# Kernel tuning notes

Hardware: AMD Instinct MI355X
Metric: run time of the kernel (lower is better)

## Reference

```python
import jax, jax.numpy as jnp
import numpy as np

TGT, SRC, BATCH, HID, ATT = 64, 64, 32, 512, 512

def setup_inputs() -> dict:
    key = jax.random.key(0)
    k1, k2, k3, k4 = jax.random.split(key, 4)
    h_t = jax.random.normal(k1, (TGT, BATCH, HID), dtype=jnp.float32)
    src_encodings = jax.random.normal(k2, (SRC, BATCH, HID), dtype=jnp.float32)
    # Wa: Linear(2*HID -> ATT, bias=False); stored as (in, out) for jnp.
    Wa = jax.random.normal(k3, (2 * HID, ATT), dtype=jnp.float32) * (1.0 / np.sqrt(2 * HID))
    # Va: Linear(ATT -> 1, bias=False)
    Va = jax.random.normal(k4, (ATT,), dtype=jnp.float32) * (1.0 / np.sqrt(ATT))
    return {"h_t": h_t, "src_encodings": src_encodings, "Wa": Wa, "Va": Va}

def reference(h_t, src_encodings, Wa, Va):
    # Wa([h_t, src]) = h_t @ Wa_h + src @ Wa_s (exact by linearity of concat-matmul)
    Wa_h, Wa_s = Wa[:HID], Wa[HID:]                 # (H, A) each
    h_part = jnp.einsum('tbh,ha->tba', h_t, Wa_h)   # (T, B, A)
    s_part = jnp.einsum('sbh,ha->sba', src_encodings, Wa_s)  # (S, B, A)
    # scores[s, t, b] = Va . tanh(h_part[t,b] + s_part[s,b])
    hidden = jnp.tanh(h_part[None, :, :, :] + s_part[:, None, :, :])  # (S, T, B, A)
    scores = jnp.einsum('stba,a->stb', hidden, Va)  # (S, T, B)
    attn = jax.nn.softmax(scores, axis=0)           # softmax over src dim
    # context[t,b,:] = sum_s attn[s,t,b] * src[s,b,:]
    context = jnp.einsum('stb,sbh->tbh', attn, src_encodings)  # (T, B, H)
    return context
```

## Files before the change

### kernel.cpp

```cpp
#include <hip/hip_runtime.h>
#include <hip/hip_bf16.h>

#define TGT   64
#define SRCN  64
#define BATCH 32
#define HID   512
#define ATT   512
#define MROWS (TGT * BATCH)

typedef __bf16 bf16_t;
typedef __bf16 bf16x8 __attribute__((ext_vector_type(8)));
typedef float  f32x4  __attribute__((ext_vector_type(4)));

__device__ __forceinline__ float fast_exp2(float x) {
#if __has_builtin(__builtin_amdgcn_exp2f)
  return __builtin_amdgcn_exp2f(x);
#else
  float r; asm("v_exp_f32 %0, %1\n\ts_nop 1" : "=v"(r) : "v"(x)); return r;
#endif
}
__device__ __forceinline__ float fast_rcp(float x) {
#if __has_builtin(__builtin_amdgcn_rcpf)
  return __builtin_amdgcn_rcpf(x);
#else
  float r; asm("v_rcp_f32 %0, %1\n\ts_nop 1" : "=v"(r) : "v"(x)); return r;
#endif
}

#define MFMA(a, b, c) __builtin_amdgcn_mfma_f32_16x16x32_bf16((a), (b), (c), 0, 0, 0)

__global__ __launch_bounds__(256) void proj_gemm(
    const float* __restrict__ h_t, const float* __restrict__ srcp,
    const float* __restrict__ Wa, float* __restrict__ C)
{
  const int z = blockIdx.z;
  const float* __restrict__ A = z ? srcp : h_t;
  const int mbase = blockIdx.x * 64;
  const int nbase = blockIdx.y * 64;

  __shared__ bf16_t Ah[64][72];
  __shared__ bf16_t Al[64][72];
  __shared__ bf16_t Bh[64][72];
  __shared__ bf16_t Bl[64][72];

  const int tid  = threadIdx.x;
  const int lane = tid & 63;
  const int wv   = tid >> 6;
  const int wm   = (wv & 1) * 32;
  const int wn   = (wv >> 1) * 32;
  const int l15  = lane & 15;
  const int qd   = lane >> 4;

  const int arow = tid >> 2;
  const int akc  = (tid & 3) * 16;
  const int bn = tid & 63;
  const int bkg = (tid >> 6) * 16;

  const float* Aptr = A + (size_t)(mbase + arow) * HID + akc;
  const float* Bptr = Wa + (size_t)(z * HID + bkg) * ATT + nbase + bn;

  f32x4 acc00 = {0.f, 0.f, 0.f, 0.f};
  f32x4 acc01 = acc00, acc10 = acc00, acc11 = acc00;

  for (int kb = 0; kb < HID; kb += 64) {
    if (kb) __syncthreads();

    {
      float4 a0 = *(const float4*)(Aptr + kb);
      float4 a1 = *(const float4*)(Aptr + kb + 4);
      float4 a2 = *(const float4*)(Aptr + kb + 8);
      float4 a3 = *(const float4*)(Aptr + kb + 12);
      float av[16] = {a0.x, a0.y, a0.z, a0.w, a1.x, a1.y, a1.z, a1.w,
                      a2.x, a2.y, a2.z, a2.w, a3.x, a3.y, a3.z, a3.w};
      bf16x8 hi0, hi1, lo0, lo1;
#pragma unroll
      for (int j = 0; j < 8; ++j) {
        bf16_t h = (bf16_t)av[j];
        hi0[j] = h;
        lo0[j] = (bf16_t)(av[j] - (float)h);
        bf16_t h2 = (bf16_t)av[j + 8];
        hi1[j] = h2;
        lo1[j] = (bf16_t)(av[j + 8] - (float)h2);
      }
      *(bf16x8*)&Ah[arow][akc]     = hi0;
      *(bf16x8*)&Ah[arow][akc + 8] = hi1;
      *(bf16x8*)&Al[arow][akc]     = lo0;
      *(bf16x8*)&Al[arow][akc + 8] = lo1;
    }

    {
      const float* bp = Bptr + (size_t)kb * ATT;
      float bv[16];
#pragma unroll
      for (int j = 0; j < 16; ++j) bv[j] = bp[(size_t)j * ATT];
      bf16x8 hi0, hi1, lo0, lo1;
#pragma unroll
      for (int j = 0; j < 8; ++j) {
        bf16_t h = (bf16_t)bv[j];
        hi0[j] = h;
        lo0[j] = (bf16_t)(bv[j] - (float)h);
        bf16_t h2 = (bf16_t)bv[j + 8];
        hi1[j] = h2;
        lo1[j] = (bf16_t)(bv[j + 8] - (float)h2);
      }
      *(bf16x8*)&Bh[bn][bkg]     = hi0;
      *(bf16x8*)&Bh[bn][bkg + 8] = hi1;
      *(bf16x8*)&Bl[bn][bkg]     = lo0;
      *(bf16x8*)&Bl[bn][bkg + 8] = lo1;
    }
    __syncthreads();

#pragma unroll
    for (int h = 0; h < 2; ++h) {
      const int kh = h * 32 + qd * 8;
      bf16x8 ah0 = *(const bf16x8*)&Ah[wm + l15][kh];
      bf16x8 ah1 = *(const bf16x8*)&Ah[wm + 16 + l15][kh];
      bf16x8 al0 = *(const bf16x8*)&Al[wm + l15][kh];
      bf16x8 al1 = *(const bf16x8*)&Al[wm + 16 + l15][kh];
      bf16x8 bh0 = *(const bf16x8*)&Bh[wn + l15][kh];
      bf16x8 bh1 = *(const bf16x8*)&Bh[wn + 16 + l15][kh];
      bf16x8 bl0 = *(const bf16x8*)&Bl[wn + l15][kh];
      bf16x8 bl1 = *(const bf16x8*)&Bl[wn + 16 + l15][kh];

      acc00 = MFMA(ah0, bh0, acc00);
      acc01 = MFMA(ah0, bh1, acc01);
      acc10 = MFMA(ah1, bh0, acc10);
      acc11 = MFMA(ah1, bh1, acc11);
      acc00 = MFMA(al0, bh0, acc00);
      acc01 = MFMA(al0, bh1, acc01);
      acc10 = MFMA(al1, bh0, acc10);
      acc11 = MFMA(al1, bh1, acc11);
      acc00 = MFMA(ah0, bl0, acc00);
      acc01 = MFMA(ah0, bl1, acc01);
      acc10 = MFMA(ah1, bl0, acc10);
      acc11 = MFMA(ah1, bl1, acc11);
    }
  }

  float* Cz = C + (size_t)z * (MROWS * ATT);
#pragma unroll
  for (int r = 0; r < 4; ++r) {
    int row0 = mbase + wm + qd * 4 + r;
    int row1 = row0 + 16;
    int col0 = nbase + wn + l15;
    Cz[(size_t)row0 * ATT + col0]      = acc00[r];
    Cz[(size_t)row0 * ATT + col0 + 16] = acc01[r];
    Cz[(size_t)row1 * ATT + col0]      = acc10[r];
    Cz[(size_t)row1 * ATT + col0 + 16] = acc11[r];
  }
}

__global__ __launch_bounds__(512) void attn_fused(
    const float* __restrict__ ws, const float* __restrict__ srcp,
    const float* __restrict__ Va, float* __restrict__ out)
{
  const float* __restrict__ h_part = ws;
  const float* __restrict__ s_part = ws + (size_t)TGT * BATCH * ATT;
  const float SC = 2.8853900817779268f;

  const int t0   = blockIdx.x * 4;
  const int b    = blockIdx.y;
  const int tid  = threadIdx.x;
  const int lane = tid & 63;
  const int wv   = tid >> 6;

  __shared__ float scoreLds[4][64];
  __shared__ float attnLds[4][64];

  const int abase = lane * 8;
  float va[8], H[4][8];
  *(float4*)&va[0] = *(const float4*)(Va + abase);
  *(float4*)&va[4] = *(const float4*)(Va + abase + 4);

  float vsum = 0.f;
#pragma unroll
  for (int j = 0; j < 8; ++j) vsum += va[j];
#pragma unroll
  for (int off = 32; off; off >>= 1) vsum += __shfl_xor(vsum, off);

#pragma unroll
  for (int t = 0; t < 4; ++t) {
    const float* hp = h_part + ((size_t)(t0 + t) * BATCH + b) * ATT + abase;
    float4 h0 = *(const float4*)hp;
    float4 h1 = *(const float4*)(hp + 4);
    H[t][0] = h0.x * SC; H[t][1] = h0.y * SC; H[t][2] = h0.z * SC; H[t][3] = h0.w * SC;
    H[t][4] = h1.x * SC; H[t][5] = h1.y * SC; H[t][6] = h1.z * SC; H[t][7] = h1.w * SC;
  }

#pragma unroll 2
  for (int i = 0; i < 8; ++i) {
    const int s = wv * 8 + i;
    const float* sp = s_part + ((size_t)s * BATCH + b) * ATT + abase;
    float4 s0 = *(const float4*)sp;
    float4 s1 = *(const float4*)(sp + 4);
    float sv[8] = {s0.x * SC, s0.y * SC, s0.z * SC, s0.w * SC,
                   s1.x * SC, s1.y * SC, s1.z * SC, s1.w * SC};
    float q0 = 0.f, q1 = 0.f, q2 = 0.f, q3 = 0.f;
#pragma unroll
    for (int j = 0; j < 8; ++j) {
      float xv = sv[j];
      float vj = va[j];
      q0 = fmaf(vj, fast_rcp(fast_exp2(xv + H[0][j]) + 1.0f), q0);
      q1 = fmaf(vj, fast_rcp(fast_exp2(xv + H[1][j]) + 1.0f), q1);
      q2 = fmaf(vj, fast_rcp(fast_exp2(xv + H[2][j]) + 1.0f), q2);
      q3 = fmaf(vj, fast_rcp(fast_exp2(xv + H[3][j]) + 1.0f), q3);
    }
#pragma unroll
    for (int off = 32; off; off >>= 1) {
      q0 += __shfl_xor(q0, off);
      q1 += __shfl_xor(q1, off);
      q2 += __shfl_xor(q2, off);
      q3 += __shfl_xor(q3, off);
    }
    if (lane == 0) {
      scoreLds[0][s] = vsum - 2.0f * q0;
      scoreLds[1][s] = vsum - 2.0f * q1;
      scoreLds[2][s] = vsum - 2.0f * q2;
      scoreLds[3][s] = vsum - 2.0f * q3;
    }
  }
  __syncthreads();

  if (wv < 4) {
    float sc = scoreLds[wv][lane];
    float m = sc;
#pragma unroll
    for (int off = 32; off; off >>= 1) m = fmaxf(m, __shfl_xor(m, off));
    float e = fast_exp2((sc - m) * 1.4426950408889634f);
    float ssum = e;
#pragma unroll
    for (int off = 32; off; off >>= 1) ssum += __shfl_xor(ssum, off);
    attnLds[wv][lane] = e * fast_rcp(ssum);
  }
  __syncthreads();

  {
    float c0 = 0.f, c1 = 0.f, c2 = 0.f, c3 = 0.f;
    const float* sb = srcp + (size_t)b * HID + tid;
#pragma unroll 8
    for (int s = 0; s < SRCN; ++s) {
      float sv = sb[(size_t)s * BATCH * HID];
      c0 = fmaf(attnLds[0][s], sv, c0);
      c1 = fmaf(attnLds[1][s], sv, c1);
      c2 = fmaf(attnLds[2][s], sv, c2);
      c3 = fmaf(attnLds[3][s], sv, c3);
    }
    out[((size_t)(t0 + 0) * BATCH + b) * HID + tid] = c0;
    out[((size_t)(t0 + 1) * BATCH + b) * HID + tid] = c1;
    out[((size_t)(t0 + 2) * BATCH + b) * HID + tid] = c2;
    out[((size_t)(t0 + 3) * BATCH + b) * HID + tid] = c3;
  }
}

extern "C" void kernel_launch(void* const* d_in, const int* in_sizes, int n_in,
                              void* d_out, int out_size, void* d_ws, size_t ws_size,
                              hipStream_t stream) {
  const float* h_t = (const float*)d_in[0];
  const float* src = (const float*)d_in[1];
  const float* Wa  = (const float*)d_in[2];
  const float* Va  = (const float*)d_in[3];
  float* out = (float*)d_out;
  float* C   = (float*)d_ws;

  proj_gemm<<<dim3(32, 8, 2), 256, 0, stream>>>(h_t, src, Wa, C);
  attn_fused<<<dim3(16, 32), 512, 0, stream>>>(C, src, Va, out);
}
```

Before: 100.3 us.

## Factor tanh exponentials separately and pair reciprocals in attention scoring

The attention kernel now precomputes exp2 of the scaled h and s projections separately, so each tanh term becomes 1/(1+eh*es). This removes one exp per (s,t,a) element, and two such terms share a single reciprocal. The projection GEMM folds in the scale, writes its output in batch-major order, and issues its global loads before the bf16 conversion. Each block now handles 8 targets, with partial sums reduced through LDS. Products of exponentials risk overflow or precision loss for large inputs.

```diff
diff --git a/kernel.cpp b/kernel.cpp
--- a/kernel.cpp
+++ b/kernel.cpp
@@ -65,11 +65,16 @@
   for (int kb = 0; kb < HID; kb += 64) {
     if (kb) __syncthreads();
 
+    float4 a0 = *(const float4*)(Aptr + kb);
+    float4 a1 = *(const float4*)(Aptr + kb + 4);
+    float4 a2 = *(const float4*)(Aptr + kb + 8);
+    float4 a3 = *(const float4*)(Aptr + kb + 12);
+    const float* bp = Bptr + (size_t)kb * ATT;
+    float bv[16];
+#pragma unroll
+    for (int j = 0; j < 16; ++j) bv[j] = bp[(size_t)j * ATT];
+
     {
-      float4 a0 = *(const float4*)(Aptr + kb);
-      float4 a1 = *(const float4*)(Aptr + kb + 4);
-      float4 a2 = *(const float4*)(Aptr + kb + 8);
-      float4 a3 = *(const float4*)(Aptr + kb + 12);
       float av[16] = {a0.x, a0.y, a0.z, a0.w, a1.x, a1.y, a1.z, a1.w,
                       a2.x, a2.y, a2.z, a2.w, a3.x, a3.y, a3.z, a3.w};
       bf16x8 hi0, hi1, lo0, lo1;
@@ -87,12 +92,7 @@
       *(bf16x8*)&Al[arow][akc]     = lo0;
       *(bf16x8*)&Al[arow][akc + 8] = lo1;
     }
-
     {
-      const float* bp = Bptr + (size_t)kb * ATT;
-      float bv[16];
-#pragma unroll
-      for (int j = 0; j < 16; ++j) bv[j] = bp[(size_t)j * ATT];
       bf16x8 hi0, hi1, lo0, lo1;
 #pragma unroll
       for (int j = 0; j < 8; ++j) {
@@ -137,16 +137,19 @@
     }
   }
 
+  const float SC = 2.8853900817779268f;
   float* Cz = C + (size_t)z * (MROWS * ATT);
 #pragma unroll
   for (int r = 0; r < 4; ++r) {
-    int row0 = mbase + wm + qd * 4 + r;
-    int row1 = row0 + 16;
+    int m0 = mbase + wm + qd * 4 + r;
+    int m1 = m0 + 16;
+    int row0 = (m0 & 31) * 64 + (m0 >> 5);
+    int row1 = (m1 & 31) * 64 + (m1 >> 5);
     int col0 = nbase + wn + l15;
-    Cz[(size_t)row0 * ATT + col0]      = acc00[r];
-    Cz[(size_t)row0 * ATT + col0 + 16] = acc01[r];
-    Cz[(size_t)row1 * ATT + col0]      = acc10[r];
-    Cz[(size_t)row1 * ATT + col0 + 16] = acc11[r];
+    Cz[(size_t)row0 * ATT + col0]      = acc00[r] * SC;
+    Cz[(size_t)row0 * ATT + col0 + 16] = acc01[r] * SC;
+    Cz[(size_t)row1 * ATT + col0]      = acc10[r] * SC;
+    Cz[(size_t)row1 * ATT + col0 + 16] = acc11[r] * SC;
   }
 }
 
@@ -156,99 +159,134 @@
 {
   const float* __restrict__ h_part = ws;
   const float* __restrict__ s_part = ws + (size_t)TGT * BATCH * ATT;
-  const float SC = 2.8853900817779268f;
-
-  const int t0   = blockIdx.x * 4;
-  const int b    = blockIdx.y;
+
+  const int bid  = blockIdx.x;
+  const int b    = bid >> 3;
+  const int t0   = (bid & 7) * 8;
   const int tid  = threadIdx.x;
   const int lane = tid & 63;
   const int wv   = tid >> 6;
 
-  __shared__ float scoreLds[4][64];
-  __shared__ float attnLds[4][64];
-
-  const int abase = lane * 8;
-  float va[8], H[4][8];
-  *(float4*)&va[0] = *(const float4*)(Va + abase);
-  *(float4*)&va[4] = *(const float4*)(Va + abase + 4);
+  __shared__ float EHs[512][12];
+  __shared__ float EsW[8][16][65];
+  __shared__ float partialQ[8][8][64];
+  __shared__ float attnT[64][12];
+  __shared__ float wsumLds[8];
+
+  {
+    float myva = Va[tid];
+    float v = myva;
+#pragma unroll
+    for (int off = 32; off; off >>= 1) v += __shfl_xor(v, off);
+    if (lane == 0) wsumLds[wv] = v;
+    EHs[tid][8] = myva;
+#pragma unroll
+    for (int t = 0; t < 8; ++t) {
+      float hv = h_part[(size_t)(b * 64 + t0 + t) * ATT + tid];
+      EHs[tid][t] = fast_exp2(hv);
+    }
+  }
+  __syncthreads();
 
   float vsum = 0.f;
 #pragma unroll
-  for (int j = 0; j < 8; ++j) vsum += va[j];
-#pragma unroll
-  for (int off = 32; off; off >>= 1) vsum += __shfl_xor(vsum, off);
-
-#pragma unroll
-  for (int t = 0; t < 4; ++t) {
-    const float* hp = h_part + ((size_t)(t0 + t) * BATCH + b) * ATT + abase;
-    float4 h0 = *(const float4*)hp;
-    float4 h1 = *(const float4*)(hp + 4);
-    H[t][0] = h0.x * SC; H[t][1] = h0.y * SC; H[t][2] = h0.z * SC; H[t][3] = h0.w * SC;
-    H[t][4] = h1.x * SC; H[t][5] = h1.y * SC; H[t][6] = h1.z * SC; H[t][7] = h1.w * SC;
-  }
-
-#pragma unroll 2
-  for (int i = 0; i < 8; ++i) {
-    const int s = wv * 8 + i;
-    const float* sp = s_part + ((size_t)s * BATCH + b) * ATT + abase;
-    float4 s0 = *(const float4*)sp;
-    float4 s1 = *(const float4*)(sp + 4);
-    float sv[8] = {s0.x * SC, s0.y * SC, s0.z * SC, s0.w * SC,
-                   s1.x * SC, s1.y * SC, s1.z * SC, s1.w * SC};
-    float q0 = 0.f, q1 = 0.f, q2 = 0.f, q3 = 0.f;
-#pragma unroll
-    for (int j = 0; j < 8; ++j) {
-      float xv = sv[j];
-      float vj = va[j];
-      q0 = fmaf(vj, fast_rcp(fast_exp2(xv + H[0][j]) + 1.0f), q0);
-      q1 = fmaf(vj, fast_rcp(fast_exp2(xv + H[1][j]) + 1.0f), q1);
-      q2 = fmaf(vj, fast_rcp(fast_exp2(xv + H[2][j]) + 1.0f), q2);
-      q3 = fmaf(vj, fast_rcp(fast_exp2(xv + H[3][j]) + 1.0f), q3);
-    }
-#pragma unroll
-    for (int off = 32; off; off >>= 1) {
-      q0 += __shfl_xor(q0, off);
-      q1 += __shfl_xor(q1, off);
-      q2 += __shfl_xor(q2, off);
-      q3 += __shfl_xor(q3, off);
-    }
-    if (lane == 0) {
-      scoreLds[0][s] = vsum - 2.0f * q0;
-      scoreLds[1][s] = vsum - 2.0f * q1;
-      scoreLds[2][s] = vsum - 2.0f * q2;
-      scoreLds[3][s] = vsum - 2.0f * q3;
-    }
-  }
+  for (int w = 0; w < 8; ++w) vsum += wsumLds[w];
+
+  float q0 = 0.f, q1 = 0.f, q2 = 0.f, q3 = 0.f;
+  float q4 = 0.f, q5 = 0.f, q6 = 0.f, q7 = 0.f;
+  const int sstg = lane >> 4;
+  const int astg = lane & 15;
+
+  for (int c = 0; c < 4; ++c) {
+    const int aBase = wv * 64 + c * 16;
+#pragma unroll
+    for (int k = 0; k < 16; ++k) {
+      int s = k * 4 + sstg;
+      float x = s_part[(size_t)(b * 64 + s) * ATT + aBase + astg];
+      EsW[wv][astg][s] = fast_exp2(x);
+    }
+#pragma unroll
+    for (int i = 0; i < 16; ++i) {
+      float e = EsW[wv][i][lane];
+      const int a = aBase + i;
+      float4 eh0 = *(const float4*)&EHs[a][0];
+      float4 eh1 = *(const float4*)&EHs[a][4];
+      float vaa  = EHs[a][8];
+      float y0 = fmaf(e, eh0.x, 1.f);
+      float y1 = fmaf(e, eh0.y, 1.f);
+      float y2 = fmaf(e, eh0.z, 1.f);
+      float y3 = fmaf(e, eh0.w, 1.f);
+      float y4 = fmaf(e, eh1.x, 1.f);
+      float y5 = fmaf(e, eh1.y, 1.f);
+      float y6 = fmaf(e, eh1.z, 1.f);
+      float y7 = fmaf(e, eh1.w, 1.f);
+      float r01 = fast_rcp(y0 * y1);
+      float r23 = fast_rcp(y2 * y3);
+      float r45 = fast_rcp(y4 * y5);
+      float r67 = fast_rcp(y6 * y7);
+      q0 = fmaf(vaa * y1, r01, q0);
+      q1 = fmaf(vaa * y0, r01, q1);
+      q2 = fmaf(vaa * y3, r23, q2);
+      q3 = fmaf(vaa * y2, r23, q3);
+      q4 = fmaf(vaa * y5, r45, q4);
+      q5 = fmaf(vaa * y4, r45, q5);
+      q6 = fmaf(vaa * y7, r67, q6);
+      q7 = fmaf(vaa * y6, r67, q7);
+    }
+  }
+
+  partialQ[wv][0][lane] = q0;
+  partialQ[wv][1][lane] = q1;
+  partialQ[wv][2][lane] = q2;
+  partialQ[wv][3][lane] = q3;
+  partialQ[wv][4][lane] = q4;
+  partialQ[wv][5][lane] = q5;
+  partialQ[wv][6][lane] = q6;
+  partialQ[wv][7][lane] = q7;
   __syncthreads();
 
-  if (wv < 4) {
-    float sc = scoreLds[wv][lane];
-    float m = sc;
+  {
+    float s_acc = 0.f;
+#pragma unroll
+    for (int w = 0; w < 8; ++w) s_acc += partialQ[w][wv][lane];
+    float score = vsum - 2.f * s_acc;
+    float m = score;
 #pragma unroll
     for (int off = 32; off; off >>= 1) m = fmaxf(m, __shfl_xor(m, off));
-    float e = fast_exp2((sc - m) * 1.4426950408889634f);
+    float e = fast_exp2((score - m) * 1.4426950408889634f);
     float ssum = e;
 #pragma unroll
     for (int off = 32; off; off >>= 1) ssum += __shfl_xor(ssum, off);
-    attnLds[wv][lane] = e * fast_rcp(ssum);
+    attnT[lane][wv] = e * fast_rcp(ssum);
   }
   __syncthreads();
 
   {
     float c0 = 0.f, c1 = 0.f, c2 = 0.f, c3 = 0.f;
+    float c4 = 0.f, c5 = 0.f, c6 = 0.f, c7 = 0.f;
     const float* sb = srcp + (size_t)b * HID + tid;
-#pragma unroll 8
+#pragma unroll 4
     for (int s = 0; s < SRCN; ++s) {
       float sv = sb[(size_t)s * BATCH * HID];
-      c0 = fmaf(attnLds[0][s], sv, c0);
-      c1 = fmaf(attnLds[1][s], sv, c1);
-      c2 = fmaf(attnLds[2][s], sv, c2);
-      c3 = fmaf(attnLds[3][s], sv, c3);
+      float4 a0 = *(const float4*)&attnT[s][0];
+      float4 a1 = *(const float4*)&attnT[s][4];
+      c0 = fmaf(a0.x, sv, c0);
+      c1 = fmaf(a0.y, sv, c1);
+      c2 = fmaf(a0.z, sv, c2);
+      c3 = fmaf(a0.w, sv, c3);
+      c4 = fmaf(a1.x, sv, c4);
+      c5 = fmaf(a1.y, sv, c5);
+      c6 = fmaf(a1.z, sv, c6);
+      c7 = fmaf(a1.w, sv, c7);
     }
     out[((size_t)(t0 + 0) * BATCH + b) * HID + tid] = c0;
     out[((size_t)(t0 + 1) * BATCH + b) * HID + tid] = c1;
     out[((size_t)(t0 + 2) * BATCH + b) * HID + tid] = c2;
     out[((size_t)(t0 + 3) * BATCH + b) * HID + tid] = c3;
+    out[((size_t)(t0 + 4) * BATCH + b) * HID + tid] = c4;
+    out[((size_t)(t0 + 5) * BATCH + b) * HID + tid] = c5;
+    out[((size_t)(t0 + 6) * BATCH + b) * HID + tid] = c6;
+    out[((size_t)(t0 + 7) * BATCH + b) * HID + tid] = c7;
   }
 }
 
@@ -263,5 +301,5 @@
   float* C   = (float*)d_ws;
 
   proj_gemm<<<dim3(32, 8, 2), 256, 0, stream>>>(h_t, src, Wa, C);
-  attn_fused<<<dim3(16, 32), 512, 0, stream>>>(C, src, Va, out);
-}
+  attn_fused<<<256, 512, 0, stream>>>(C, src, Va, out);
+}
```

Result: slower. 103.9 us (+3.6%).
